# Kernel optimization log

Hardware: AMD Instinct MI355X
Metric: run time of the kernel (lower is better)

Reference implementation:

```python
import jax, jax.numpy as jnp
import numpy as np

B, T, HID = 2, 2048, 2048
NH, NKV, HD = 32, 8, 64
SCALE = HD ** -0.5
ROPE_THETA = 10000.0


def _rope_tables(key):
    # standard HF llama rope: cos/sin of shape [B, T, head_dim]
    inv_freq = 1.0 / (ROPE_THETA ** (jnp.arange(0, HD, 2, dtype=jnp.float32) / HD))
    pos = jnp.arange(T, dtype=jnp.float32)
    freqs = pos[:, None] * inv_freq[None, :]            # [T, HD/2]
    emb = jnp.concatenate([freqs, freqs], axis=-1)      # [T, HD]
    cos = jnp.broadcast_to(jnp.cos(emb)[None], (B, T, HD))
    sin = jnp.broadcast_to(jnp.sin(emb)[None], (B, T, HD))
    return cos, sin


def setup_inputs() -> dict:
    key = jax.random.key(0)
    ks = jax.random.split(key, 5)
    hidden_states = jax.random.normal(ks[0], (B, T, HID), dtype=jnp.float32)
    cos, sin = _rope_tables(key)
    s = 0.02
    wq = jax.random.normal(ks[1], (NH * HD, HID), dtype=jnp.float32) * s
    wk = jax.random.normal(ks[2], (NKV * HD, HID), dtype=jnp.float32) * s
    wv = jax.random.normal(ks[3], (NKV * HD, HID), dtype=jnp.float32) * s
    wo = jax.random.normal(ks[4], (HID, NH * HD), dtype=jnp.float32) * s
    return {"hidden_states": hidden_states, "cos": cos, "sin": sin,
            "wq": wq, "wk": wk, "wv": wv, "wo": wo}


def _rotate_half(x):
    x1, x2 = jnp.split(x, 2, axis=-1)
    return jnp.concatenate([-x2, x1], axis=-1)


def _apply_rope(q, k, cos, sin):
    # q: [B, NH, T, HD], k: [B, NKV, T, HD]; cos/sin: [B, T, HD] -> unsqueeze head dim
    c = cos[:, None, :, :]
    s = sin[:, None, :, :]
    q = q * c + _rotate_half(q) * s
    k = k * c + _rotate_half(k) * s
    return q, k


def reference(hidden_states, cos, sin, wq, wk, wv, wo):
    b, t, _ = hidden_states.shape
    # QKV projections (no bias, llama-style)
    q = (hidden_states @ wq.T).reshape(b, t, NH, HD).transpose(0, 2, 1, 3)    # [B,NH,T,HD]
    k = (hidden_states @ wk.T).reshape(b, t, NKV, HD).transpose(0, 2, 1, 3)   # [B,NKV,T,HD]
    v = (hidden_states @ wv.T).reshape(b, t, NKV, HD).transpose(0, 2, 1, 3)
    q, k = _apply_rope(q, k, cos, sin)
    # GQA: repeat kv heads
    rep = NH // NKV
    k = jnp.repeat(k, rep, axis=1)   # [B,NH,T,HD]
    v = jnp.repeat(v, rep, axis=1)
    # causal attention, scaling = head_dim**-0.5
    logits = jnp.einsum("bhqd,bhkd->bhqk", q, k) * SCALE
    causal = jnp.tril(jnp.ones((t, t), dtype=bool))
    logits = jnp.where(causal[None, None], logits, jnp.finfo(logits.dtype).min)
    probs = jax.nn.softmax(logits, axis=-1)
    attn = jnp.einsum("bhqk,bhkd->bhqd", probs, v)       # [B,NH,T,HD]
    attn = attn.transpose(0, 2, 1, 3).reshape(b, t, NH * HD)
    return attn @ wo.T
```

## Files before the change

kernel.cpp:

```cpp
#include <hip/hip_runtime.h>
#include <hip/hip_bf16.h>

#define T_SEQ 2048
#define HID_DIM 2048

typedef __attribute__((ext_vector_type(8))) short short8;
typedef __attribute__((ext_vector_type(4))) float f32x4;

#define MFMA16(a, b, c) __builtin_amdgcn_mfma_f32_16x16x32_bf16((a), (b), (c), 0, 0, 0)

static __device__ __forceinline__ ushort f2bf(float f) {
  union { __hip_bfloat16 h; ushort u; } un;
  un.h = __float2bfloat16(f);
  return un.u;
}
static __device__ __forceinline__ float bf2f(ushort u) {
  union { ushort u; __hip_bfloat16 h; } un;
  un.u = u;
  return __bfloat162float(un.h);
}

static __device__ __forceinline__ void gload_lds16(const void* g, void* l) {
  __builtin_amdgcn_global_load_lds(
      (const __attribute__((address_space(1))) void*)g,
      (__attribute__((address_space(3))) void*)l, 16, 0, 0);
}

__global__ __launch_bounds__(256) void cast_kernel(const float* __restrict__ in,
                                                   ushort* __restrict__ out, int n4) {
  int i = blockIdx.x * 256 + threadIdx.x;
  if (i >= n4) return;
  const float4 v = reinterpret_cast<const float4*>(in)[i];
  ushort4 o;
  o.x = f2bf(v.x); o.y = f2bf(v.y); o.z = f2bf(v.z); o.w = f2bf(v.w);
  reinterpret_cast<ushort4*>(out)[i] = o;
}

__device__ __forceinline__ void store_c(float* p, float v) { *p = v; }
__device__ __forceinline__ void store_c(ushort* p, float v) { *p = f2bf(v); }

template <int MODE, typename OutT>
__global__ __launch_bounds__(256) void gemm_bt(const ushort* __restrict__ A,
                                               const ushort* __restrict__ W,
                                               OutT* __restrict__ C,
                                               ushort* __restrict__ vTout,
                                               int M, int N, int K) {
  __shared__ __align__(16) ushort As[128][32];
  __shared__ __align__(16) ushort Bs[128][32];
  const int brow = blockIdx.y * 128, bcol = blockIdx.x * 128;
  const int tid = threadIdx.x;
  const int wid = tid >> 6, lane = tid & 63, l15 = lane & 15, lhi = lane >> 4;
  const int wr = wid >> 1, wc = wid & 1;
  const int srow = tid >> 2, scol = (tid & 3) * 8;

  f32x4 acc[4][4] = {};

  const ushort* a0 = A + (size_t)(brow + srow) * K + scol;
  const ushort* a1 = A + (size_t)(brow + 64 + srow) * K + scol;
  const ushort* w0 = W + (size_t)(bcol + srow) * K + scol;
  const ushort* w1 = W + (size_t)(bcol + 64 + srow) * K + scol;
  ushort* lA0 = &As[0][0] + tid * 8;
  ushort* lA1 = &As[0][0] + 2048 + tid * 8;
  ushort* lB0 = &Bs[0][0] + tid * 8;
  ushort* lB1 = &Bs[0][0] + 2048 + tid * 8;

  for (int k0 = 0; k0 < K; k0 += 32) {
    gload_lds16(a0 + k0, lA0);
    gload_lds16(a1 + k0, lA1);
    gload_lds16(w0 + k0, lB0);
    gload_lds16(w1 + k0, lB1);
    __syncthreads();
    short8 af[4], bfr[4];
#pragma unroll
    for (int m = 0; m < 4; ++m)
      af[m] = *(const short8*)&As[wr * 64 + m * 16 + l15][lhi * 8];
#pragma unroll
    for (int n = 0; n < 4; ++n)
      bfr[n] = *(const short8*)&Bs[wc * 64 + n * 16 + l15][lhi * 8];
#pragma unroll
    for (int m = 0; m < 4; ++m)
#pragma unroll
      for (int n = 0; n < 4; ++n)
        acc[m][n] = MFMA16(af[m], bfr[n], acc[m][n]);
    __syncthreads();
  }

  if (MODE == 2 && bcol >= 2560) {
#pragma unroll
    for (int m = 0; m < 4; ++m) {
      const int row = brow + wr * 64 + m * 16 + lhi * 4;
      const int bb = row >> 11, t = row & 2047;
#pragma unroll
      for (int n = 0; n < 4; ++n) {
        const int cv = bcol + wc * 64 + n * 16 + l15 - 2560;
        const int hk = cv >> 6, dd = cv & 63;
        ushort4 o;
        o.x = f2bf(acc[m][n][0]); o.y = f2bf(acc[m][n][1]);
        o.z = f2bf(acc[m][n][2]); o.w = f2bf(acc[m][n][3]);
        *(ushort4*)&vTout[(size_t)((bb * 8 + hk) * 64 + dd) * 2048 + t] = o;
      }
    }
  } else {
    const int cstride = (MODE == 2) ? 2560 : N;
#pragma unroll
    for (int m = 0; m < 4; ++m) {
      const int row = brow + wr * 64 + m * 16 + lhi * 4;
#pragma unroll
      for (int n = 0; n < 4; ++n) {
        const int col = bcol + wc * 64 + n * 16 + l15;
#pragma unroll
        for (int r = 0; r < 4; ++r)
          store_c(&C[(size_t)(row + r) * cstride + col], acc[m][n][r]);
      }
    }
  }
}

__global__ __launch_bounds__(256) void rope_kernel(ushort* __restrict__ qkv,
                                                   const float* __restrict__ ct,
                                                   const float* __restrict__ st) {
  const int bt = blockIdx.x;
  ushort* row = qkv + (size_t)bt * 2560;
  const float* c = ct + (size_t)bt * 64;
  const float* s = st + (size_t)bt * 64;
  const int tid = threadIdx.x;
#pragma unroll
  for (int it = 0; it < 5; ++it) {
    const int idx = it * 256 + tid;
    const bool isQ = idx < 1024;
    const int sub = isQ ? idx : idx - 1024;
    const int hh = sub >> 5;
    const int p = sub & 31;
    const int col = (isQ ? 0 : 2048) + hh * 64 + p;
    const float x1 = bf2f(row[col]);
    const float x2 = bf2f(row[col + 32]);
    const float cc = c[p], ss = s[p];
    float y1 = x1 * cc - x2 * ss;
    float y2 = x2 * cc + x1 * ss;
    if (isQ) { y1 *= 0.125f; y2 *= 0.125f; }
    row[col] = f2bf(y1);
    row[col + 32] = f2bf(y2);
  }
}

#define PROCESS(SUF, diag_) do {                                              \
    const size_t qoff_ =                                                      \
        (size_t)(b * T_SEQ + q##SUF * 64 + wid * 16 + l15) * 2560 + h * 64 +  \
        lhi * 8;                                                              \
    const short8 q0_ = *(const short8*)(qkv + qoff_);                         \
    const short8 q1_ = *(const short8*)(qkv + qoff_ + 32);                    \
    f32x4 s_[4] = {};                                                         \
    _Pragma("unroll")                                                         \
    for (int n = 0; n < 4; ++n) {                                             \
      const int kv = n * 16 + l15;                                            \
      const int sw = (kv & 7) << 4;                                           \
      const short8 k0_ = *(const short8*)((const char*)Kt + kv * 128 + ((lhi * 16) ^ sw));      \
      const short8 k1_ = *(const short8*)((const char*)Kt + kv * 128 + ((64 + lhi * 16) ^ sw)); \
      s_[n] = MFMA16(q0_, k0_, s_[n]);                                        \
      s_[n] = MFMA16(q1_, k1_, s_[n]);                                        \
    }                                                                         \
    _Pragma("unroll")                                                         \
    for (int r = 0; r < 4; ++r) {                                             \
      const int qrl = wid * 16 + lhi * 4 + r;                                 \
      if (diag_) {                                                            \
        _Pragma("unroll")                                                     \
        for (int n = 0; n < 4; ++n)                                           \
          if (n * 16 + l15 > qrl) s_[n][r] = -1e30f;                          \
      }                                                                       \
      float mx = fmaxf(fmaxf(s_[0][r], s_[1][r]), fmaxf(s_[2][r], s_[3][r])); \
      mx = fmaxf(mx, __shfl_xor(mx, 1));                                      \
      mx = fmaxf(mx, __shfl_xor(mx, 2));                                      \
      mx = fmaxf(mx, __shfl_xor(mx, 4));                                      \
      mx = fmaxf(mx, __shfl_xor(mx, 8));                                      \
      const float mn = fmaxf(m##SUF[r], mx);                                  \
      const float al = __expf(m##SUF[r] - mn);                                \
      float rs = 0.f;                                                         \
      _Pragma("unroll")                                                       \
      for (int n = 0; n < 4; ++n) {                                           \
        const float p_ = __expf(s_[n][r] - mn);                               \
        s_[n][r] = p_;                                                        \
        rs += p_;                                                             \
      }                                                                       \
      rs += __shfl_xor(rs, 1); rs += __shfl_xor(rs, 2);                       \
      rs += __shfl_xor(rs, 4); rs += __shfl_xor(rs, 8);                       \
      l##SUF[r] = l##SUF[r] * al + rs;                                        \
      m##SUF[r] = mn;                                                         \
      _Pragma("unroll")                                                       \
      for (int n = 0; n < 4; ++n) {                                           \
        o##SUF[n][r] *= al;                                                   \
        Pt[qrl][n * 16 + l15] = f2bf(s_[n][r]);                               \
      }                                                                       \
    }                                                                         \
    {                                                                         \
      const short8 p0_ = *(const short8*)&Pt[wid * 16 + l15][lhi * 8];        \
      const short8 p1_ = *(const short8*)&Pt[wid * 16 + l15][32 + lhi * 8];   \
      _Pragma("unroll")                                                       \
      for (int n = 0; n < 4; ++n) {                                           \
        const int dv = n * 16 + l15;                                          \
        const int sw = (dv & 7) << 4;                                         \
        const short8 v0_ = *(const short8*)((const char*)Vt + dv * 128 + ((lhi * 16) ^ sw));      \
        const short8 v1_ = *(const short8*)((const char*)Vt + dv * 128 + ((64 + lhi * 16) ^ sw)); \
        o##SUF[n] = MFMA16(p0_, v0_, o##SUF[n]);                              \
        o##SUF[n] = MFMA16(p1_, v1_, o##SUF[n]);                              \
      }                                                                       \
    }                                                                         \
  } while (0)

__global__ __launch_bounds__(256) void attn_kernel(const ushort* __restrict__ qkv,
                                                   const ushort* __restrict__ vT,
                                                   ushort* __restrict__ out) {
  __shared__ __align__(16) ushort Kt[4096];
  __shared__ __align__(16) ushort Vt[4096];
  __shared__ __align__(16) ushort Pt[64][72];
  const int bid = blockIdx.x;
  const int j = bid >> 3;
  const int bh = (bid & 7) * 8 + (j & 7);
  const int bx = j >> 3;
  const int b = bh >> 5, h = bh & 31, hkv = h >> 2;
  const int tid = threadIdx.x;
  const int wid = tid >> 6, lane = tid & 63, l15 = lane & 15, lhi = lane >> 4;
  const int qA = bx, qB = 31 - bx;

  f32x4 oA[4] = {}, oB[4] = {};
  float mA[4], lA[4], mB[4], lB[4];
#pragma unroll
  for (int r = 0; r < 4; ++r) { mA[r] = mB[r] = -1e30f; lA[r] = lB[r] = 0.f; }

  const int srow = tid >> 3, sgrp = tid & 7;
  const int d0s = ((sgrp ^ (srow & 7)) * 8);
  const ushort* kb_g = qkv + (size_t)b * T_SEQ * 2560 + 2048 + hkv * 64;
  const ushort* vb_g = vT + (size_t)(b * 8 + hkv) * 64 * 2048;
  ushort* ldsK = Kt + tid * 8;
  ushort* ldsV = Vt + tid * 8;

  for (int kt = 0; kt <= qB; ++kt) {
    const int ktb = kt * 64;
    gload_lds16(kb_g + (size_t)(ktb + srow) * 2560 + d0s, ldsK);
    gload_lds16(kb_g + (size_t)(ktb + 32 + srow) * 2560 + d0s, ldsK + 2048);
    gload_lds16(vb_g + (size_t)srow * 2048 + ktb + d0s, ldsV);
    gload_lds16(vb_g + (size_t)(32 + srow) * 2048 + ktb + d0s, ldsV + 2048);
    __syncthreads();
    PROCESS(B, kt == qB);
    if (kt <= qA) PROCESS(A, kt == qA);
    __syncthreads();
  }

#pragma unroll
  for (int r = 0; r < 4; ++r) {
    const float invA = 1.f / lA[r];
    const size_t orowA = (size_t)(b * T_SEQ + qA * 64 + wid * 16 + lhi * 4 + r);
#pragma unroll
    for (int n = 0; n < 4; ++n)
      out[orowA * 2048 + h * 64 + n * 16 + l15] = f2bf(oA[n][r] * invA);
  }
#pragma unroll
  for (int r = 0; r < 4; ++r) {
    const float invB = 1.f / lB[r];
    const size_t orowB = (size_t)(b * T_SEQ + qB * 64 + wid * 16 + lhi * 4 + r);
#pragma unroll
    for (int n = 0; n < 4; ++n)
      out[orowB * 2048 + h * 64 + n * 16 + l15] = f2bf(oB[n][r] * invB);
  }
}

extern "C" void kernel_launch(void* const* d_in, const int* in_sizes, int n_in,
                              void* d_out, int out_size, void* d_ws, size_t ws_size,
                              hipStream_t stream) {
  const float* hs   = (const float*)d_in[0];
  const float* cosb = (const float*)d_in[1];
  const float* sinb = (const float*)d_in[2];
  const float* wq   = (const float*)d_in[3];
  const float* wk   = (const float*)d_in[4];
  const float* wv   = (const float*)d_in[5];
  const float* wo   = (const float*)d_in[6];
  float* out = (float*)d_out;

  char* ws = (char*)d_ws;
  ushort* hsb   = (ushort*)(ws);
  ushort* wqkvb = (ushort*)(ws + 16777216);
  ushort* wob   = (ushort*)(ws + 29360128);
  ushort* qkvQK = (ushort*)(ws + 37748736);
  ushort* vTb   = (ushort*)(ws + 58720256);
  ushort* attno = hsb;

  cast_kernel<<<8192, 256, 0, stream>>>(hs, hsb, 2097152);
  cast_kernel<<<4096, 256, 0, stream>>>(wq, wqkvb, 1048576);
  cast_kernel<<<1024, 256, 0, stream>>>(wk, wqkvb + 4194304, 262144);
  cast_kernel<<<1024, 256, 0, stream>>>(wv, wqkvb + 5242880, 262144);
  cast_kernel<<<4096, 256, 0, stream>>>(wo, wob, 1048576);

  gemm_bt<2, ushort><<<dim3(24, 32), 256, 0, stream>>>(hsb, wqkvb, qkvQK, vTb,
                                                       4096, 3072, 2048);

  rope_kernel<<<4096, 256, 0, stream>>>(qkvQK, cosb, sinb);

  attn_kernel<<<1024, 256, 0, stream>>>(qkvQK, vTb, attno);

  gemm_bt<0, float><<<dim3(16, 32), 256, 0, stream>>>(attno, wob, out, nullptr,
                                                      4096, 2048, 2048);
}
```

Baseline: 384.7 us.

## Compute transposed S=K·Q^T so softmax rows reduce in-lane; hoist Q loads

The QK^T MFMA now swaps its operands so each lane holds scores for a single query row across several keys. The row max and sum then need only two cross-lane shuffles per row instead of four shuffles for each of four rows, and P is written to LDS as packed 4-element vectors rather than scalar stores. Q fragments are loaded once into registers before the KV loop instead of on every tile, and s_setprio raises wave priority around the MFMA sections. The rescale factors now have to be broadcast with __shfl to match the O accumulator layout, which adds some shuffle work.

```diff
diff --git a/kernel.cpp b/kernel.cpp
--- a/kernel.cpp
+++ b/kernel.cpp
@@ -5,6 +5,7 @@
 #define HID_DIM 2048
 
 typedef __attribute__((ext_vector_type(8))) short short8;
+typedef __attribute__((ext_vector_type(4))) short short4v;
 typedef __attribute__((ext_vector_type(4))) float f32x4;
 
 #define MFMA16(a, b, c) __builtin_amdgcn_mfma_f32_16x16x32_bf16((a), (b), (c), 0, 0, 0)
@@ -144,65 +145,88 @@
 }
 
 #define PROCESS(SUF, diag_) do {                                              \
-    const size_t qoff_ =                                                      \
-        (size_t)(b * T_SEQ + q##SUF * 64 + wid * 16 + l15) * 2560 + h * 64 +  \
-        lhi * 8;                                                              \
-    const short8 q0_ = *(const short8*)(qkv + qoff_);                         \
-    const short8 q1_ = *(const short8*)(qkv + qoff_ + 32);                    \
     f32x4 s_[4] = {};                                                         \
+    __builtin_amdgcn_s_setprio(1);                                            \
     _Pragma("unroll")                                                         \
     for (int n = 0; n < 4; ++n) {                                             \
-      const int kv = n * 16 + l15;                                            \
-      const int sw = (kv & 7) << 4;                                           \
-      const short8 k0_ = *(const short8*)((const char*)Kt + kv * 128 + ((lhi * 16) ^ sw));      \
-      const short8 k1_ = *(const short8*)((const char*)Kt + kv * 128 + ((64 + lhi * 16) ^ sw)); \
-      s_[n] = MFMA16(q0_, k0_, s_[n]);                                        \
-      s_[n] = MFMA16(q1_, k1_, s_[n]);                                        \
-    }                                                                         \
-    _Pragma("unroll")                                                         \
-    for (int r = 0; r < 4; ++r) {                                             \
-      const int qrl = wid * 16 + lhi * 4 + r;                                 \
-      if (diag_) {                                                            \
-        _Pragma("unroll")                                                     \
-        for (int n = 0; n < 4; ++n)                                           \
-          if (n * 16 + l15 > qrl) s_[n][r] = -1e30f;                          \
-      }                                                                       \
-      float mx = fmaxf(fmaxf(s_[0][r], s_[1][r]), fmaxf(s_[2][r], s_[3][r])); \
-      mx = fmaxf(mx, __shfl_xor(mx, 1));                                      \
-      mx = fmaxf(mx, __shfl_xor(mx, 2));                                      \
-      mx = fmaxf(mx, __shfl_xor(mx, 4));                                      \
-      mx = fmaxf(mx, __shfl_xor(mx, 8));                                      \
-      const float mn = fmaxf(m##SUF[r], mx);                                  \
-      const float al = __expf(m##SUF[r] - mn);                                \
-      float rs = 0.f;                                                         \
+      const short8 k0_ = *(const short8*)(KtB + n * 2048 + base0);            \
+      const short8 k1_ = *(const short8*)(KtB + n * 2048 + base1);            \
+      s_[n] = MFMA16(k0_, q##SUF##0, s_[n]);                                  \
+      s_[n] = MFMA16(k1_, q##SUF##1, s_[n]);                                  \
+    }                                                                         \
+    __builtin_amdgcn_s_setprio(0);                                            \
+    if (diag_) {                                                              \
       _Pragma("unroll")                                                       \
       for (int n = 0; n < 4; ++n) {                                           \
-        const float p_ = __expf(s_[n][r] - mn);                               \
-        s_[n][r] = p_;                                                        \
-        rs += p_;                                                             \
+        const int kb_ = 16 * n + 4 * lhi;                                     \
+        _Pragma("unroll")                                                     \
+        for (int r = 0; r < 4; ++r)                                           \
+          if (kb_ + r > qloc) s_[n][r] = -1e30f;                              \
       }                                                                       \
-      rs += __shfl_xor(rs, 1); rs += __shfl_xor(rs, 2);                       \
-      rs += __shfl_xor(rs, 4); rs += __shfl_xor(rs, 8);                       \
-      l##SUF[r] = l##SUF[r] * al + rs;                                        \
-      m##SUF[r] = mn;                                                         \
+    }                                                                         \
+    float mx_;                                                                \
+    {                                                                         \
+      const float m0_ = fmaxf(fmaxf(s_[0][0], s_[0][1]), fmaxf(s_[0][2], s_[0][3])); \
+      const float m1_ = fmaxf(fmaxf(s_[1][0], s_[1][1]), fmaxf(s_[1][2], s_[1][3])); \
+      const float m2_ = fmaxf(fmaxf(s_[2][0], s_[2][1]), fmaxf(s_[2][2], s_[2][3])); \
+      const float m3_ = fmaxf(fmaxf(s_[3][0], s_[3][1]), fmaxf(s_[3][2], s_[3][3])); \
+      mx_ = fmaxf(fmaxf(m0_, m1_), fmaxf(m2_, m3_));                          \
+    }                                                                         \
+    mx_ = fmaxf(mx_, __shfl_xor(mx_, 16));                                    \
+    mx_ = fmaxf(mx_, __shfl_xor(mx_, 32));                                    \
+    const float mn_ = fmaxf(mS##SUF, mx_);                                    \
+    const float al_ = __expf(mS##SUF - mn_);                                  \
+    _Pragma("unroll")                                                         \
+    for (int n = 0; n < 4; ++n) {                                             \
+      s_[n][0] = __expf(s_[n][0] - mn_);                                      \
+      s_[n][1] = __expf(s_[n][1] - mn_);                                      \
+      s_[n][2] = __expf(s_[n][2] - mn_);                                      \
+      s_[n][3] = __expf(s_[n][3] - mn_);                                      \
+    }                                                                         \
+    float rs_;                                                                \
+    {                                                                         \
+      const float t0_ = (s_[0][0] + s_[0][1]) + (s_[0][2] + s_[0][3]);        \
+      const float t1_ = (s_[1][0] + s_[1][1]) + (s_[1][2] + s_[1][3]);        \
+      const float t2_ = (s_[2][0] + s_[2][1]) + (s_[2][2] + s_[2][3]);        \
+      const float t3_ = (s_[3][0] + s_[3][1]) + (s_[3][2] + s_[3][3]);        \
+      rs_ = (t0_ + t1_) + (t2_ + t3_);                                        \
+    }                                                                         \
+    rs_ += __shfl_xor(rs_, 16);                                               \
+    rs_ += __shfl_xor(rs_, 32);                                               \
+    lS##SUF = lS##SUF * al_ + rs_;                                            \
+    mS##SUF = mn_;                                                            \
+    _Pragma("unroll")                                                         \
+    for (int n = 0; n < 4; ++n) {                                             \
+      short4v pk_;                                                            \
+      pk_[0] = (short)f2bf(s_[n][0]);                                         \
+      pk_[1] = (short)f2bf(s_[n][1]);                                         \
+      pk_[2] = (short)f2bf(s_[n][2]);                                         \
+      pk_[3] = (short)f2bf(s_[n][3]);                                         \
+      *(short4v*)(PtB + prow + 32 * n + 8 * lhi) = pk_;                       \
+    }                                                                         \
+    const float al0_ = __shfl(al_, 4 * lhi + 0);                              \
+    const float al1_ = __shfl(al_, 4 * lhi + 1);                              \
+    const float al2_ = __shfl(al_, 4 * lhi + 2);                              \
+    const float al3_ = __shfl(al_, 4 * lhi + 3);                              \
+    _Pragma("unroll")                                                         \
+    for (int n = 0; n < 4; ++n) {                                             \
+      o##SUF[n][0] *= al0_;                                                   \
+      o##SUF[n][1] *= al1_;                                                   \
+      o##SUF[n][2] *= al2_;                                                   \
+      o##SUF[n][3] *= al3_;                                                   \
+    }                                                                         \
+    {                                                                         \
+      const short8 p0_ = *(const short8*)(PtB + prow + 16 * lhi);             \
+      const short8 p1_ = *(const short8*)(PtB + prow + 64 + 16 * lhi);        \
+      __builtin_amdgcn_s_setprio(1);                                          \
       _Pragma("unroll")                                                       \
       for (int n = 0; n < 4; ++n) {                                           \
-        o##SUF[n][r] *= al;                                                   \
-        Pt[qrl][n * 16 + l15] = f2bf(s_[n][r]);                               \
-      }                                                                       \
-    }                                                                         \
-    {                                                                         \
-      const short8 p0_ = *(const short8*)&Pt[wid * 16 + l15][lhi * 8];        \
-      const short8 p1_ = *(const short8*)&Pt[wid * 16 + l15][32 + lhi * 8];   \
-      _Pragma("unroll")                                                       \
-      for (int n = 0; n < 4; ++n) {                                           \
-        const int dv = n * 16 + l15;                                          \
-        const int sw = (dv & 7) << 4;                                         \
-        const short8 v0_ = *(const short8*)((const char*)Vt + dv * 128 + ((lhi * 16) ^ sw));      \
-        const short8 v1_ = *(const short8*)((const char*)Vt + dv * 128 + ((64 + lhi * 16) ^ sw)); \
+        const short8 v0_ = *(const short8*)(VtB + n * 2048 + base0);          \
+        const short8 v1_ = *(const short8*)(VtB + n * 2048 + base1);          \
         o##SUF[n] = MFMA16(p0_, v0_, o##SUF[n]);                              \
         o##SUF[n] = MFMA16(p1_, v1_, o##SUF[n]);                              \
       }                                                                       \
+      __builtin_amdgcn_s_setprio(0);                                          \
     }                                                                         \
   } while (0)
 
@@ -211,7 +235,7 @@
                                                    ushort* __restrict__ out) {
   __shared__ __align__(16) ushort Kt[4096];
   __shared__ __align__(16) ushort Vt[4096];
-  __shared__ __align__(16) ushort Pt[64][72];
+  __shared__ __align__(16) ushort Pt[64 * 72];
   const int bid = blockIdx.x;
   const int j = bid >> 3;
   const int bh = (bid & 7) * 8 + (j & 7);
@@ -220,11 +244,28 @@
   const int tid = threadIdx.x;
   const int wid = tid >> 6, lane = tid & 63, l15 = lane & 15, lhi = lane >> 4;
   const int qA = bx, qB = 31 - bx;
+  const int qloc = wid * 16 + l15;
+
+  short8 qA0, qA1, qB0, qB1;
+  {
+    const size_t offA = (size_t)(b * T_SEQ + qA * 64 + qloc) * 2560 + h * 64;
+    qA0 = *(const short8*)(qkv + offA + lhi * 8);
+    qA1 = *(const short8*)(qkv + offA + 32 + lhi * 8);
+    const size_t offB = (size_t)(b * T_SEQ + qB * 64 + qloc) * 2560 + h * 64;
+    qB0 = *(const short8*)(qkv + offB + lhi * 8);
+    qB1 = *(const short8*)(qkv + offB + 32 + lhi * 8);
+  }
 
   f32x4 oA[4] = {}, oB[4] = {};
-  float mA[4], lA[4], mB[4], lB[4];
-#pragma unroll
-  for (int r = 0; r < 4; ++r) { mA[r] = mB[r] = -1e30f; lA[r] = lB[r] = 0.f; }
+  float mSA = -1e30f, lSA = 0.f, mSB = -1e30f, lSB = 0.f;
+
+  const int swb = (l15 & 7) << 4;
+  const int base0 = l15 * 128 + ((lhi * 16) ^ swb);
+  const int base1 = l15 * 128 + ((64 + lhi * 16) ^ swb);
+  const char* KtB = (const char*)Kt;
+  const char* VtB = (const char*)Vt;
+  char* PtB = (char*)Pt;
+  const int prow = qloc * 144;
 
   const int srow = tid >> 3, sgrp = tid & 7;
   const int d0s = ((sgrp ^ (srow & 7)) * 8);
@@ -245,21 +286,31 @@
     __syncthreads();
   }
 
-#pragma unroll
-  for (int r = 0; r < 4; ++r) {
-    const float invA = 1.f / lA[r];
-    const size_t orowA = (size_t)(b * T_SEQ + qA * 64 + wid * 16 + lhi * 4 + r);
-#pragma unroll
-    for (int n = 0; n < 4; ++n)
-      out[orowA * 2048 + h * 64 + n * 16 + l15] = f2bf(oA[n][r] * invA);
-  }
-#pragma unroll
-  for (int r = 0; r < 4; ++r) {
-    const float invB = 1.f / lB[r];
-    const size_t orowB = (size_t)(b * T_SEQ + qB * 64 + wid * 16 + lhi * 4 + r);
-#pragma unroll
-    for (int n = 0; n < 4; ++n)
-      out[orowB * 2048 + h * 64 + n * 16 + l15] = f2bf(oB[n][r] * invB);
+  {
+    const float invA = 1.f / lSA;
+    const float i0 = __shfl(invA, 4 * lhi + 0), i1 = __shfl(invA, 4 * lhi + 1);
+    const float i2 = __shfl(invA, 4 * lhi + 2), i3 = __shfl(invA, 4 * lhi + 3);
+    const size_t orow = (size_t)(b * T_SEQ + qA * 64 + wid * 16 + lhi * 4);
+#pragma unroll
+    for (int n = 0; n < 4; ++n) {
+      out[(orow + 0) * 2048 + h * 64 + n * 16 + l15] = f2bf(oA[n][0] * i0);
+      out[(orow + 1) * 2048 + h * 64 + n * 16 + l15] = f2bf(oA[n][1] * i1);
+      out[(orow + 2) * 2048 + h * 64 + n * 16 + l15] = f2bf(oA[n][2] * i2);
+      out[(orow + 3) * 2048 + h * 64 + n * 16 + l15] = f2bf(oA[n][3] * i3);
+    }
+  }
+  {
+    const float invB = 1.f / lSB;
+    const float i0 = __shfl(invB, 4 * lhi + 0), i1 = __shfl(invB, 4 * lhi + 1);
+    const float i2 = __shfl(invB, 4 * lhi + 2), i3 = __shfl(invB, 4 * lhi + 3);
+    const size_t orow = (size_t)(b * T_SEQ + qB * 64 + wid * 16 + lhi * 4);
+#pragma unroll
+    for (int n = 0; n < 4; ++n) {
+      out[(orow + 0) * 2048 + h * 64 + n * 16 + l15] = f2bf(oB[n][0] * i0);
+      out[(orow + 1) * 2048 + h * 64 + n * 16 + l15] = f2bf(oB[n][1] * i1);
+      out[(orow + 2) * 2048 + h * 64 + n * 16 + l15] = f2bf(oB[n][2] * i2);
+      out[(orow + 3) * 2048 + h * 64 + n * 16 + l15] = f2bf(oB[n][3] * i3);
+    }
   }
 }
 
```

Result: faster. 341.8 us (-11.2%).
